# Kernel tuning notes

Measured on AMD Instinct MI355X. Metric: run time of the kernel, lower is better.

Reference implementation:

```python
import jax, jax.numpy as jnp
import numpy as np

D_MODEL = 2048
N_HEADS = 16
N_KV_HEADS = 4
D_K = D_MODEL // N_HEADS  # 128
N_REP = N_HEADS // N_KV_HEADS  # 4
EPS = 1e-8
ROPE_BASE = 10000.0


def setup_inputs() -> dict:
    key = jax.random.key(0)
    ks = jax.random.split(key, 6)
    B, S = 2, 2048
    s_in = 1.0 / np.sqrt(D_MODEL)
    return {
        "x": jax.random.normal(ks[0], (B, S, D_MODEL), jnp.float32),
        "Wq": jax.random.normal(ks[1], (D_MODEL, D_MODEL), jnp.float32) * s_in,
        "bq": jnp.zeros((D_MODEL,), jnp.float32),
        "Wk": jax.random.normal(ks[2], (N_KV_HEADS * D_K, D_MODEL), jnp.float32) * s_in,
        "bk": jnp.zeros((N_KV_HEADS * D_K,), jnp.float32),
        "Wv": jax.random.normal(ks[3], (N_KV_HEADS * D_K, D_MODEL), jnp.float32) * s_in,
        "bv": jnp.zeros((N_KV_HEADS * D_K,), jnp.float32),
        "Wo": jax.random.normal(ks[4], (D_MODEL, D_MODEL), jnp.float32) * s_in,
        "bo": jnp.zeros((D_MODEL,), jnp.float32),
        "q_norm_w": jnp.ones((D_K,), jnp.float32),
        "k_norm_w": jnp.ones((D_K,), jnp.float32),
    }


def _rmsnorm(x, w):
    rms = jnp.sqrt(jnp.mean(x * x, axis=-1, keepdims=True) + EPS)
    return x / rms * w


def _rope(x, cos, sin):
    # x: [B, S, H, d_k]; interleaved pair rotation (pairs along last dim)
    B, S, H, d = x.shape
    xr = x.reshape(B, S, H, d // 2, 2)
    x1, x2 = xr[..., 0], xr[..., 1]
    c = cos[:, None, :]  # [S, 1, d/2] -> broadcasts over [B, S, H, d/2]
    s = sin[:, None, :]
    o1 = x1 * c - x2 * s
    o2 = x1 * s + x2 * c
    return jnp.stack([o1, o2], axis=-1).reshape(B, S, H, d)


def reference(x, Wq, bq, Wk, bk, Wv, bv, Wo, bo, q_norm_w, k_norm_w):
    B, S, D = x.shape
    scale = 1.0 / np.sqrt(D_K)

    q = (x @ Wq.T + bq).reshape(B, S, N_HEADS, D_K)
    k = (x @ Wk.T + bk).reshape(B, S, N_KV_HEADS, D_K)
    v = (x @ Wv.T + bv).reshape(B, S, N_KV_HEADS, D_K)

    q = _rmsnorm(q, q_norm_w)
    k = _rmsnorm(k, k_norm_w)

    # RoPE tables (cos/sin of t * inv_freq), shape [S, d_k/2]
    inv_freq = 1.0 / (ROPE_BASE ** (jnp.arange(0, D_K, 2, dtype=jnp.float32) / D_K))
    freqs = jnp.arange(S, dtype=jnp.float32)[:, None] * inv_freq[None, :]
    cos, sin = jnp.cos(freqs), jnp.sin(freqs)
    q = _rope(q, cos, sin)
    k = _rope(k, cos, sin)

    # [B, H, S, d]
    q = q.transpose(0, 2, 1, 3)
    k = k.transpose(0, 2, 1, 3)
    v = v.transpose(0, 2, 1, 3)

    # GQA: group q heads by kv head instead of repeating k/v
    qg = q.reshape(B, N_KV_HEADS, N_REP, S, D_K)
    scores = jnp.einsum("bkrqd,bkld->bkrql", qg, k) * scale
    causal = jnp.tril(jnp.ones((S, S), dtype=bool))  # [S, S]
    scores = jnp.where(causal, scores, jnp.float32(-1e9))
    attn = jax.nn.softmax(scores, axis=-1)
    out = jnp.einsum("bkrql,bkld->bkrqd", attn, v)  # [B, Hk, rep, S, d]
    out = out.reshape(B, N_HEADS, S, D_K).transpose(0, 2, 1, 3).reshape(B, S, D)
    return out @ Wo.T + bo
```

## Files before the change

### kernel.cpp

```cpp
#include <hip/hip_runtime.h>
#include <hip/hip_bf16.h>
#include <stdint.h>

#define DM 2048
#define SQ 2048
#define NB 2
#define NH 16
#define NKV 4
#define DK 128
#define NQKV 3072

typedef unsigned short u16;
typedef unsigned int u32;
typedef __attribute__((ext_vector_type(8))) __bf16 bf16x8;
typedef __attribute__((ext_vector_type(4))) float f32x4;
typedef __attribute__((ext_vector_type(8))) u16 u16x8;
typedef __attribute__((ext_vector_type(2))) u32 u32x2;

__device__ __forceinline__ u16 f2bf(float f) {
  u32 x = __builtin_bit_cast(u32, f);
  x += 0x7fffu + ((x >> 16) & 1u);
  return (u16)(x >> 16);
}

__device__ __forceinline__ f32x4 mfma16(bf16x8 a, bf16x8 b, f32x4 c) {
  return __builtin_amdgcn_mfma_f32_16x16x32_bf16(a, b, c, 0, 0, 0);
}

#define GLDS16(g, l)                                                          \
  __builtin_amdgcn_global_load_lds(                                           \
      (const __attribute__((address_space(1))) void*)(g),                     \
      (__attribute__((address_space(3))) void*)(l), 16, 0, 0)

__global__ void cast_kernel(const float* __restrict__ src, u16* __restrict__ dst, int n8) {
  int i = blockIdx.x * blockDim.x + threadIdx.x;
  if (i >= n8) return;
  const float4* s4 = (const float4*)src;
  float4 a = s4[2 * i], b = s4[2 * i + 1];
  u16x8 v;
  v[0] = f2bf(a.x); v[1] = f2bf(a.y); v[2] = f2bf(a.z); v[3] = f2bf(a.w);
  v[4] = f2bf(b.x); v[5] = f2bf(b.y); v[6] = f2bf(b.z); v[7] = f2bf(b.w);
  *(u16x8*)(dst + 8 * (size_t)i) = v;
}

__global__ void fuse_bias(const float* __restrict__ bq, const float* __restrict__ bk,
                          const float* __restrict__ bv, float* __restrict__ fb) {
  int i = blockIdx.x * blockDim.x + threadIdx.x;
  if (i >= NQKV) return;
  float v;
  if (i < DM) v = bq[i];
  else if (i < DM + NKV * DK) v = bk[i - DM];
  else v = bv[i - DM - NKV * DK];
  fb[i] = v;
}

__global__ __launch_bounds__(256) void gemm_bt(
    const u16* __restrict__ A, const u16* __restrict__ W,
    const float* __restrict__ bias, float* __restrict__ C,
    int M, int N, int K) {
  __shared__ u16 As[128 * 64];
  __shared__ u16 Bs[128 * 64];
  const int tid = threadIdx.x;
  const int w = tid >> 6, l = tid & 63;
  const int hi = l >> 4, lo = l & 15;
  const int MB = M >> 7;
  const int nwg = gridDim.x;
  const int bid = blockIdx.x;
  const int swz = (bid & 7) * (nwg >> 3) + (bid >> 3);
  const int bm = swz % MB, bn = swz / MB;
  const int wr = w >> 1, wc = w & 1;
  const int lr8 = l >> 3, lc = l & 7;
  f32x4 acc[4][4] = {};
  for (int kt = 0; kt < K; kt += 64) {
#pragma unroll
    for (int i = 0; i < 4; ++i) {
      int row = w * 32 + i * 8 + lr8;
      int gc = lc ^ (row & 7);
      GLDS16(A + (size_t)(bm * 128 + row) * K + kt + gc * 8, &As[(w * 32 + i * 8) * 64]);
    }
#pragma unroll
    for (int i = 0; i < 4; ++i) {
      int row = w * 32 + i * 8 + lr8;
      int gc = lc ^ (row & 7);
      GLDS16(W + (size_t)(bn * 128 + row) * K + kt + gc * 8, &Bs[(w * 32 + i * 8) * 64]);
    }
    __syncthreads();
#pragma unroll
    for (int kk = 0; kk < 2; ++kk) {
      bf16x8 af[4], bf[4];
#pragma unroll
      for (int mi = 0; mi < 4; ++mi) {
        int row = wr * 64 + mi * 16 + lo;
        af[mi] = *(const bf16x8*)&As[row * 64 + (((kk * 4 + hi) ^ (row & 7)) * 8)];
      }
#pragma unroll
      for (int ni = 0; ni < 4; ++ni) {
        int row = wc * 64 + ni * 16 + lo;
        bf[ni] = *(const bf16x8*)&Bs[row * 64 + (((kk * 4 + hi) ^ (row & 7)) * 8)];
      }
#pragma unroll
      for (int mi = 0; mi < 4; ++mi)
#pragma unroll
        for (int ni = 0; ni < 4; ++ni)
          acc[mi][ni] = mfma16(af[mi], bf[ni], acc[mi][ni]);
    }
    __syncthreads();
  }
#pragma unroll
  for (int mi = 0; mi < 4; ++mi) {
#pragma unroll
    for (int ni = 0; ni < 4; ++ni) {
      int col = bn * 128 + wc * 64 + ni * 16 + lo;
      float bv = bias[col];
#pragma unroll
      for (int r = 0; r < 4; ++r) {
        int rowg = bm * 128 + wr * 64 + mi * 16 + hi * 4 + r;
        C[(size_t)rowg * N + col] = acc[mi][ni][r] + bv;
      }
    }
  }
}

__global__ void normrope_qk(const float* __restrict__ qkv,
                            const float* __restrict__ qw, const float* __restrict__ kw,
                            u16* __restrict__ qb, u16* __restrict__ kb) {
  int gw = (int)((blockIdx.x * (size_t)blockDim.x + threadIdx.x) >> 6);
  int lane = threadIdx.x & 63;
  int bs = gw / (NH + NKV), j = gw % (NH + NKV);
  int b = bs / SQ, s = bs % SQ;
  const float* src;
  const float* wgt;
  u16* dst;
  float post = 1.0f;
  if (j < NH) {
    src = qkv + (size_t)bs * NQKV + j * DK;
    wgt = qw;
    dst = qb + ((size_t)(b * NH + j) * SQ + s) * DK;
    post = 0.08838834764831845f;
  } else {
    int kh = j - NH;
    src = qkv + (size_t)bs * NQKV + DM + kh * DK;
    wgt = kw;
    dst = kb + ((size_t)(b * NKV + kh) * SQ + s) * DK;
  }
  float2 xv = *(const float2*)(src + 2 * lane);
  float ss = xv.x * xv.x + xv.y * xv.y;
#pragma unroll
  for (int m = 1; m < 64; m <<= 1) ss += __shfl_xor(ss, m);
  float inv = rsqrtf(ss * (1.0f / DK) + 1e-8f);
  float x1 = xv.x * inv * wgt[2 * lane];
  float x2 = xv.y * inv * wgt[2 * lane + 1];
  float theta = (float)s * expf((float)lane * (-9.2103403720f / 64.0f));
  float sn, cs;
  sincosf(theta, &sn, &cs);
  float o1 = (x1 * cs - x2 * sn) * post;
  float o2 = (x1 * sn + x2 * cs) * post;
  u32 pack = (u32)f2bf(o1) | ((u32)f2bf(o2) << 16);
  *(u32*)(dst + 2 * lane) = pack;
}

__global__ __launch_bounds__(256) void vtrans(const float* __restrict__ qkv, u16* __restrict__ vt) {
  __shared__ u16 T[128 * 72];
  int bid = blockIdx.x;
  int st = bid % (SQ / 64);
  int rem = bid / (SQ / 64);
  int vh = rem % NKV, b = rem / NKV;
  int s0 = st * 64;
  int t = threadIdx.x;
#pragma unroll
  for (int it = 0; it < 8; ++it) {
    int idx = it * 256 + t;
    int sl = idx >> 5;
    int c4 = idx & 31;
    float4 v = *(const float4*)(qkv + (size_t)(b * SQ + s0 + sl) * NQKV + DM + NKV * DK + vh * DK + c4 * 4);
    T[(c4 * 4 + 0) * 72 + sl] = f2bf(v.x);
    T[(c4 * 4 + 1) * 72 + sl] = f2bf(v.y);
    T[(c4 * 4 + 2) * 72 + sl] = f2bf(v.z);
    T[(c4 * 4 + 3) * 72 + sl] = f2bf(v.w);
  }
  __syncthreads();
#pragma unroll
  for (int it = 0; it < 4; ++it) {
    int idx = it * 256 + t;
    int d = idx >> 3;
    int ch = idx & 7;
    u16x8 v = *(const u16x8*)&T[d * 72 + ch * 8];
    *(u16x8*)(vt + ((size_t)(b * NKV + vh) * DK + d) * SQ + s0 + ch * 8) = v;
  }
}

__global__ __launch_bounds__(256) void attn(const u16* __restrict__ qb, const u16* __restrict__ kb,
                                            const u16* __restrict__ vt, u16* __restrict__ out) {
  __shared__ u16 Ks[2][64 * 128];
  __shared__ u16 Vs[2][128 * 64];
  __shared__ u16 P[4][16 * 64];
  const int w = threadIdx.x >> 6, l = threadIdx.x & 63;
  const int hi = l >> 4, lo = l & 15;
  const int pr = blockIdx.x, h = blockIdx.y, b = blockIdx.z;
  const int kvh = h >> 2;
  const u16* Q = qb + (size_t)(b * NH + h) * SQ * DK;
  const u16* K = kb + (size_t)(b * NKV + kvh) * SQ * DK;
  const u16* V = vt + (size_t)(b * NKV + kvh) * DK * SQ;

  auto stageKV = [&](int buf, int kt) {
#pragma unroll
    for (int i = 0; i < 4; ++i) {
      int rb = w * 16 + i * 4;
      int row = rb + (l >> 4);
      int gc = (l & 15) ^ (row & 7);
      GLDS16(K + (size_t)(kt + row) * DK + gc * 8, &Ks[buf][rb * 128]);
    }
#pragma unroll
    for (int i = 0; i < 4; ++i) {
      int rb = w * 32 + i * 8;
      int row = rb + (l >> 3);
      int gc = (l & 7) ^ (row & 7);
      GLDS16(V + (size_t)row * SQ + kt + gc * 8, &Vs[buf][rb * 64]);
    }
  };

#pragma unroll 1
  for (int seg = 0; seg < 2; ++seg) {
    const int qt = seg ? (SQ / 64 - 1 - pr) : pr;
    const int q0 = qt * 64 + w * 16;
    bf16x8 qf[4];
#pragma unroll
    for (int kk = 0; kk < 4; ++kk)
      qf[kk] = *(const bf16x8*)(Q + (size_t)(q0 + lo) * DK + kk * 32 + hi * 8);
    f32x4 oacc[8] = {};
    float lrun = 0.f;
    const int nt = qt + 1;
    stageKV(0, 0);
    __syncthreads();
#pragma unroll 1
    for (int ti = 0; ti < nt; ++ti) {
      const int cur = ti & 1;
      if (ti + 1 < nt) stageKV(cur ^ 1, (ti + 1) * 64);
      const int kt = ti * 64;
      f32x4 sfr[4];
      __builtin_amdgcn_s_setprio(1);
#pragma unroll
      for (int cb = 0; cb < 4; ++cb) {
        f32x4 sf = {};
#pragma unroll
        for (int kk = 0; kk < 4; ++kk) {
          int row = cb * 16 + lo;
          bf16x8 kfr = *(const bf16x8*)&Ks[cur][row * 128 + (((kk * 4 + hi) ^ (row & 7)) * 8)];
          sf = mfma16(kfr, qf[kk], sf);
        }
        sfr[cb] = sf;
      }
      __builtin_amdgcn_s_setprio(0);
      if (ti == nt - 1) {
#pragma unroll
        for (int cb = 0; cb < 4; ++cb)
#pragma unroll
          for (int r = 0; r < 4; ++r) {
            int kcol = kt + cb * 16 + hi * 4 + r;
            if (kcol > q0 + lo) sfr[cb][r] = -1e9f;
          }
      }
      float rs = 0.f;
#pragma unroll
      for (int cb = 0; cb < 4; ++cb) {
        float p0 = __expf(sfr[cb][0] - 12.0f);
        float p1 = __expf(sfr[cb][1] - 12.0f);
        float p2 = __expf(sfr[cb][2] - 12.0f);
        float p3 = __expf(sfr[cb][3] - 12.0f);
        rs += (p0 + p1) + (p2 + p3);
        u32x2 pw;
        pw[0] = (u32)f2bf(p0) | ((u32)f2bf(p1) << 16);
        pw[1] = (u32)f2bf(p2) | ((u32)f2bf(p3) << 16);
        int chunk = cb * 2 + (hi >> 1);
        *(u32x2*)&P[w][lo * 64 + ((chunk ^ (lo & 7)) * 8) + (hi & 1) * 4] = pw;
      }
      rs += __shfl_xor(rs, 16);
      rs += __shfl_xor(rs, 32);
      lrun += rs;
      __builtin_amdgcn_s_setprio(1);
#pragma unroll
      for (int half = 0; half < 2; ++half) {
        bf16x8 pa = *(const bf16x8*)&P[w][lo * 64 + (((half * 4 + hi) ^ (lo & 7)) * 8)];
#pragma unroll
        for (int fr = 0; fr < 8; ++fr) {
          int row = fr * 16 + lo;
          bf16x8 vfr = *(const bf16x8*)&Vs[cur][row * 64 + (((half * 4 + hi) ^ (row & 7)) * 8)];
          oacc[fr] = mfma16(pa, vfr, oacc[fr]);
        }
      }
      __builtin_amdgcn_s_setprio(0);
      __syncthreads();
    }
    float invl = 1.0f / lrun;
    float invlB[4];
#pragma unroll
    for (int r = 0; r < 4; ++r) invlB[r] = __shfl(invl, hi * 4 + r);
#pragma unroll
    for (int fr = 0; fr < 8; ++fr) {
#pragma unroll
      for (int r = 0; r < 4; ++r) {
        int row = b * SQ + q0 + hi * 4 + r;
        int col = h * DK + fr * 16 + lo;
        out[(size_t)row * DM + col] = f2bf(oacc[fr][r] * invlB[r]);
      }
    }
  }
}

extern "C" void kernel_launch(void* const* d_in, const int* in_sizes, int n_in,
                              void* d_out, int out_size, void* d_ws, size_t ws_size,
                              hipStream_t stream) {
  const float* x = (const float*)d_in[0];
  const float* Wq = (const float*)d_in[1];
  const float* bq = (const float*)d_in[2];
  const float* Wk = (const float*)d_in[3];
  const float* bk = (const float*)d_in[4];
  const float* Wv = (const float*)d_in[5];
  const float* bv = (const float*)d_in[6];
  const float* Wo = (const float*)d_in[7];
  const float* bo = (const float*)d_in[8];
  const float* qw = (const float*)d_in[9];
  const float* kw = (const float*)d_in[10];
  float* outp = (float*)d_out;

  char* ws = (char*)d_ws;
  size_t off = 0;
  auto alloc = [&](size_t bytes) {
    char* p = ws + off;
    off += (bytes + 255) & ~(size_t)255;
    return p;
  };
  u16* xb = (u16*)alloc((size_t)NB * SQ * DM * 2);
  u16* Wqkvb = (u16*)alloc((size_t)NQKV * DM * 2);
  u16* Wob = (u16*)alloc((size_t)DM * DM * 2);
  float* fbias = (float*)alloc((size_t)NQKV * 4);
  float* qkvf = (float*)alloc((size_t)NB * SQ * NQKV * 4);
  u16* qbh = (u16*)alloc((size_t)NB * NH * SQ * DK * 2);
  u16* kbh = (u16*)alloc((size_t)NB * NKV * SQ * DK * 2);
  u16* vth = (u16*)alloc((size_t)NB * NKV * DK * SQ * 2);
  u16* aout = (u16*)alloc((size_t)NB * SQ * DM * 2);

  {
    int n8 = NB * SQ * DM / 8;
    cast_kernel<<<(n8 + 255) / 256, 256, 0, stream>>>(x, xb, n8);
    n8 = DM * DM / 8;
    cast_kernel<<<(n8 + 255) / 256, 256, 0, stream>>>(Wq, Wqkvb, n8);
    cast_kernel<<<(n8 + 255) / 256, 256, 0, stream>>>(Wo, Wob, n8);
    n8 = NKV * DK * DM / 8;
    cast_kernel<<<(n8 + 255) / 256, 256, 0, stream>>>(Wk, Wqkvb + (size_t)DM * DM, n8);
    cast_kernel<<<(n8 + 255) / 256, 256, 0, stream>>>(Wv, Wqkvb + (size_t)(DM + NKV * DK) * DM, n8);
    fuse_bias<<<(NQKV + 255) / 256, 256, 0, stream>>>(bq, bk, bv, fbias);
  }
  {
    int M = NB * SQ;
    gemm_bt<<<(M / 128) * (NQKV / 128), 256, 0, stream>>>(xb, Wqkvb, fbias, qkvf, M, NQKV, DM);
  }
  {
    int waves = NB * SQ * (NH + NKV);
    normrope_qk<<<waves / 4, 256, 0, stream>>>(qkvf, qw, kw, qbh, kbh);
    vtrans<<<NB * NKV * (SQ / 64), 256, 0, stream>>>(qkvf, vth);
  }
  {
    dim3 g(SQ / 128, NH, NB);
    attn<<<g, 256, 0, stream>>>(qbh, kbh, vth, aout);
  }
  {
    int M = NB * SQ;
    gemm_bt<<<(M / 128) * (DM / 128), 256, 0, stream>>>(aout, Wob, bo, outp, M, DM, DM);
  }
}
```

Measured before the change: 235.8 us.

## Enlarge attention query tile, merge cast kernels, precompute RoPE table, drop GEMM swizzle

The attention kernel now has each wave handle two 16-row query groups, giving 128-row query tiles. Each staged K/V tile is therefore reused across twice as many queries. Causal masking is generalised per group, and fully masked tiles are skipped. The grid shrinks to 8 blocks per head and batch, which fewer blocks may leave some CUs idle. Separately, the five cast launches become one kernel, RoPE cos/sin come from a precomputed table, and the GEMM block-index swizzle is removed, which may hurt L2 locality.

```diff
diff --git a/kernel.cpp b/kernel.cpp
--- a/kernel.cpp
+++ b/kernel.cpp
@@ -32,15 +32,25 @@
       (const __attribute__((address_space(1))) void*)(g),                     \
       (__attribute__((address_space(3))) void*)(l), 16, 0, 0)
 
-__global__ void cast_kernel(const float* __restrict__ src, u16* __restrict__ dst, int n8) {
+__global__ void cast_all(const float* __restrict__ x, const float* __restrict__ Wq,
+                         const float* __restrict__ Wk, const float* __restrict__ Wv,
+                         const float* __restrict__ Wo, u16* __restrict__ xb,
+                         u16* __restrict__ Wqkvb, u16* __restrict__ Wob) {
   int i = blockIdx.x * blockDim.x + threadIdx.x;
-  if (i >= n8) return;
+  const float* src;
+  u16* dst;
+  int j;
+  if (i < 1048576) { src = x; dst = xb; j = i; }
+  else if (i < 1572864) { src = Wq; dst = Wqkvb; j = i - 1048576; }
+  else if (i < 1703936) { src = Wk; dst = Wqkvb + (size_t)DM * DM; j = i - 1572864; }
+  else if (i < 1835008) { src = Wv; dst = Wqkvb + (size_t)(DM + NKV * DK) * DM; j = i - 1703936; }
+  else { src = Wo; dst = Wob; j = i - 1835008; }
   const float4* s4 = (const float4*)src;
-  float4 a = s4[2 * i], b = s4[2 * i + 1];
+  float4 a = s4[2 * j], b = s4[2 * j + 1];
   u16x8 v;
   v[0] = f2bf(a.x); v[1] = f2bf(a.y); v[2] = f2bf(a.z); v[3] = f2bf(a.w);
   v[4] = f2bf(b.x); v[5] = f2bf(b.y); v[6] = f2bf(b.z); v[7] = f2bf(b.w);
-  *(u16x8*)(dst + 8 * (size_t)i) = v;
+  *(u16x8*)(dst + 8 * (size_t)j) = v;
 }
 
 __global__ void fuse_bias(const float* __restrict__ bq, const float* __restrict__ bk,
@@ -52,6 +62,16 @@
   else if (i < DM + NKV * DK) v = bk[i - DM];
   else v = bv[i - DM - NKV * DK];
   fb[i] = v;
+}
+
+__global__ void rope_table(float* __restrict__ ct, float* __restrict__ st_) {
+  int i = blockIdx.x * blockDim.x + threadIdx.x;
+  int s = i >> 6, d = i & 63;
+  float theta = (float)s * __expf((float)d * (-9.2103403720f / 64.0f));
+  float sn, cs;
+  sincosf(theta, &sn, &cs);
+  ct[i] = cs;
+  st_[i] = sn;
 }
 
 __global__ __launch_bounds__(256) void gemm_bt(
@@ -64,10 +84,7 @@
   const int w = tid >> 6, l = tid & 63;
   const int hi = l >> 4, lo = l & 15;
   const int MB = M >> 7;
-  const int nwg = gridDim.x;
-  const int bid = blockIdx.x;
-  const int swz = (bid & 7) * (nwg >> 3) + (bid >> 3);
-  const int bm = swz % MB, bn = swz / MB;
+  const int bm = blockIdx.x % MB, bn = blockIdx.x / MB;
   const int wr = w >> 1, wc = w & 1;
   const int lr8 = l >> 3, lc = l & 7;
   f32x4 acc[4][4] = {};
@@ -123,6 +140,7 @@
 
 __global__ void normrope_qk(const float* __restrict__ qkv,
                             const float* __restrict__ qw, const float* __restrict__ kw,
+                            const float* __restrict__ cosT, const float* __restrict__ sinT,
                             u16* __restrict__ qb, u16* __restrict__ kb) {
   int gw = (int)((blockIdx.x * (size_t)blockDim.x + threadIdx.x) >> 6);
   int lane = threadIdx.x & 63;
@@ -150,9 +168,8 @@
   float inv = rsqrtf(ss * (1.0f / DK) + 1e-8f);
   float x1 = xv.x * inv * wgt[2 * lane];
   float x2 = xv.y * inv * wgt[2 * lane + 1];
-  float theta = (float)s * expf((float)lane * (-9.2103403720f / 64.0f));
-  float sn, cs;
-  sincosf(theta, &sn, &cs);
+  float cs = cosT[s * 64 + lane];
+  float sn = sinT[s * 64 + lane];
   float o1 = (x1 * cs - x2 * sn) * post;
   float o2 = (x1 * sn + x2 * cs) * post;
   u32 pack = (u32)f2bf(o1) | ((u32)f2bf(o2) << 16);
@@ -193,7 +210,7 @@
                                             const u16* __restrict__ vt, u16* __restrict__ out) {
   __shared__ u16 Ks[2][64 * 128];
   __shared__ u16 Vs[2][128 * 64];
-  __shared__ u16 P[4][16 * 64];
+  __shared__ u16 P[8][16 * 64];
   const int w = threadIdx.x >> 6, l = threadIdx.x & 63;
   const int hi = l >> 4, lo = l & 15;
   const int pr = blockIdx.x, h = blockIdx.y, b = blockIdx.z;
@@ -221,15 +238,17 @@
 
 #pragma unroll 1
   for (int seg = 0; seg < 2; ++seg) {
-    const int qt = seg ? (SQ / 64 - 1 - pr) : pr;
-    const int q0 = qt * 64 + w * 16;
-    bf16x8 qf[4];
-#pragma unroll
-    for (int kk = 0; kk < 4; ++kk)
-      qf[kk] = *(const bf16x8*)(Q + (size_t)(q0 + lo) * DK + kk * 32 + hi * 8);
-    f32x4 oacc[8] = {};
-    float lrun = 0.f;
-    const int nt = qt + 1;
+    const int qt = seg ? (15 - pr) : pr;
+    const int qbase = qt * 128 + w * 32;
+    bf16x8 qf[2][4];
+#pragma unroll
+    for (int g = 0; g < 2; ++g)
+#pragma unroll
+      for (int kk = 0; kk < 4; ++kk)
+        qf[g][kk] = *(const bf16x8*)(Q + (size_t)(qbase + g * 16 + lo) * DK + kk * 32 + hi * 8);
+    f32x4 oacc[2][8] = {};
+    float lrun[2] = {0.f, 0.f};
+    const int nt = 2 * qt + 2;
     stageKV(0, 0);
     __syncthreads();
 #pragma unroll 1
@@ -237,71 +256,87 @@
       const int cur = ti & 1;
       if (ti + 1 < nt) stageKV(cur ^ 1, (ti + 1) * 64);
       const int kt = ti * 64;
-      f32x4 sfr[4];
-      __builtin_amdgcn_s_setprio(1);
-#pragma unroll
-      for (int cb = 0; cb < 4; ++cb) {
-        f32x4 sf = {};
-#pragma unroll
-        for (int kk = 0; kk < 4; ++kk) {
-          int row = cb * 16 + lo;
-          bf16x8 kfr = *(const bf16x8*)&Ks[cur][row * 128 + (((kk * 4 + hi) ^ (row & 7)) * 8)];
-          sf = mfma16(kfr, qf[kk], sf);
+      if (kt <= qbase + 31) {
+        f32x4 sfr[2][4];
+        __builtin_amdgcn_s_setprio(1);
+#pragma unroll
+        for (int cb = 0; cb < 4; ++cb) {
+          f32x4 sf0 = {}, sf1 = {};
+#pragma unroll
+          for (int kk = 0; kk < 4; ++kk) {
+            int row = cb * 16 + lo;
+            bf16x8 kfr = *(const bf16x8*)&Ks[cur][row * 128 + (((kk * 4 + hi) ^ (row & 7)) * 8)];
+            sf0 = mfma16(kfr, qf[0][kk], sf0);
+            sf1 = mfma16(kfr, qf[1][kk], sf1);
+          }
+          sfr[0][cb] = sf0;
+          sfr[1][cb] = sf1;
         }
-        sfr[cb] = sf;
+        __builtin_amdgcn_s_setprio(0);
+#pragma unroll
+        for (int g = 0; g < 2; ++g) {
+          int q0 = qbase + g * 16;
+          if (kt + 63 > q0) {
+#pragma unroll
+            for (int cb = 0; cb < 4; ++cb)
+#pragma unroll
+              for (int r = 0; r < 4; ++r) {
+                int kcol = kt + cb * 16 + hi * 4 + r;
+                if (kcol > q0 + lo) sfr[g][cb][r] = -1e9f;
+              }
+          }
+        }
+#pragma unroll
+        for (int g = 0; g < 2; ++g) {
+          float rs = 0.f;
+#pragma unroll
+          for (int cb = 0; cb < 4; ++cb) {
+            float p0 = __expf(sfr[g][cb][0] - 12.0f);
+            float p1 = __expf(sfr[g][cb][1] - 12.0f);
+            float p2 = __expf(sfr[g][cb][2] - 12.0f);
+            float p3 = __expf(sfr[g][cb][3] - 12.0f);
+            rs += (p0 + p1) + (p2 + p3);
+            u32x2 pw;
+            pw[0] = (u32)f2bf(p0) | ((u32)f2bf(p1) << 16);
+            pw[1] = (u32)f2bf(p2) | ((u32)f2bf(p3) << 16);
+            int chunk = cb * 2 + (hi >> 1);
+            *(u32x2*)&P[w * 2 + g][lo * 64 + ((chunk ^ (lo & 7)) * 8) + (hi & 1) * 4] = pw;
+          }
+          rs += __shfl_xor(rs, 16);
+          rs += __shfl_xor(rs, 32);
+          lrun[g] += rs;
+        }
+        __builtin_amdgcn_s_setprio(1);
+#pragma unroll
+        for (int half = 0; half < 2; ++half) {
+          bf16x8 pa0 = *(const bf16x8*)&P[w * 2 + 0][lo * 64 + (((half * 4 + hi) ^ (lo & 7)) * 8)];
+          bf16x8 pa1 = *(const bf16x8*)&P[w * 2 + 1][lo * 64 + (((half * 4 + hi) ^ (lo & 7)) * 8)];
+#pragma unroll
+          for (int fr = 0; fr < 8; ++fr) {
+            int row = fr * 16 + lo;
+            bf16x8 vfr = *(const bf16x8*)&Vs[cur][row * 64 + (((half * 4 + hi) ^ (row & 7)) * 8)];
+            oacc[0][fr] = mfma16(pa0, vfr, oacc[0][fr]);
+            oacc[1][fr] = mfma16(pa1, vfr, oacc[1][fr]);
+          }
+        }
+        __builtin_amdgcn_s_setprio(0);
       }
-      __builtin_amdgcn_s_setprio(0);
-      if (ti == nt - 1) {
-#pragma unroll
-        for (int cb = 0; cb < 4; ++cb)
-#pragma unroll
-          for (int r = 0; r < 4; ++r) {
-            int kcol = kt + cb * 16 + hi * 4 + r;
-            if (kcol > q0 + lo) sfr[cb][r] = -1e9f;
-          }
-      }
-      float rs = 0.f;
-#pragma unroll
-      for (int cb = 0; cb < 4; ++cb) {
-        float p0 = __expf(sfr[cb][0] - 12.0f);
-        float p1 = __expf(sfr[cb][1] - 12.0f);
-        float p2 = __expf(sfr[cb][2] - 12.0f);
-        float p3 = __expf(sfr[cb][3] - 12.0f);
-        rs += (p0 + p1) + (p2 + p3);
-        u32x2 pw;
-        pw[0] = (u32)f2bf(p0) | ((u32)f2bf(p1) << 16);
-        pw[1] = (u32)f2bf(p2) | ((u32)f2bf(p3) << 16);
-        int chunk = cb * 2 + (hi >> 1);
-        *(u32x2*)&P[w][lo * 64 + ((chunk ^ (lo & 7)) * 8) + (hi & 1) * 4] = pw;
-      }
-      rs += __shfl_xor(rs, 16);
-      rs += __shfl_xor(rs, 32);
-      lrun += rs;
-      __builtin_amdgcn_s_setprio(1);
-#pragma unroll
-      for (int half = 0; half < 2; ++half) {
-        bf16x8 pa = *(const bf16x8*)&P[w][lo * 64 + (((half * 4 + hi) ^ (lo & 7)) * 8)];
-#pragma unroll
-        for (int fr = 0; fr < 8; ++fr) {
-          int row = fr * 16 + lo;
-          bf16x8 vfr = *(const bf16x8*)&Vs[cur][row * 64 + (((half * 4 + hi) ^ (row & 7)) * 8)];
-          oacc[fr] = mfma16(pa, vfr, oacc[fr]);
+      __syncthreads();
+    }
+#pragma unroll
+    for (int g = 0; g < 2; ++g) {
+      float invl = 1.0f / lrun[g];
+      float invlB[4];
+#pragma unroll
+      for (int r = 0; r < 4; ++r) invlB[r] = __shfl(invl, hi * 4 + r);
+#pragma unroll
+      for (int fr = 0; fr < 8; ++fr) {
+#pragma unroll
+        for (int r = 0; r < 4; ++r) {
+          int row = b * SQ + qbase + g * 16 + hi * 4 + r;
+          int col = h * DK + fr * 16 + lo;
+          out[(size_t)row * DM + col] = f2bf(oacc[g][fr][r] * invlB[r]);
         }
-      }
-      __builtin_amdgcn_s_setprio(0);
-      __syncthreads();
-    }
-    float invl = 1.0f / lrun;
-    float invlB[4];
-#pragma unroll
-    for (int r = 0; r < 4; ++r) invlB[r] = __shfl(invl, hi * 4 + r);
-#pragma unroll
-    for (int fr = 0; fr < 8; ++fr) {
-#pragma unroll
-      for (int r = 0; r < 4; ++r) {
-        int row = b * SQ + q0 + hi * 4 + r;
-        int col = h * DK + fr * 16 + lo;
-        out[(size_t)row * DM + col] = f2bf(oacc[fr][r] * invlB[r]);
       }
     }
   }
@@ -334,34 +369,28 @@
   u16* Wqkvb = (u16*)alloc((size_t)NQKV * DM * 2);
   u16* Wob = (u16*)alloc((size_t)DM * DM * 2);
   float* fbias = (float*)alloc((size_t)NQKV * 4);
+  float* cosT = (float*)alloc((size_t)SQ * 64 * 4);
+  float* sinT = (float*)alloc((size_t)SQ * 64 * 4);
   float* qkvf = (float*)alloc((size_t)NB * SQ * NQKV * 4);
   u16* qbh = (u16*)alloc((size_t)NB * NH * SQ * DK * 2);
   u16* kbh = (u16*)alloc((size_t)NB * NKV * SQ * DK * 2);
   u16* vth = (u16*)alloc((size_t)NB * NKV * DK * SQ * 2);
   u16* aout = (u16*)alloc((size_t)NB * SQ * DM * 2);
 
-  {
-    int n8 = NB * SQ * DM / 8;
-    cast_kernel<<<(n8 + 255) / 256, 256, 0, stream>>>(x, xb, n8);
-    n8 = DM * DM / 8;
-    cast_kernel<<<(n8 + 255) / 256, 256, 0, stream>>>(Wq, Wqkvb, n8);
-    cast_kernel<<<(n8 + 255) / 256, 256, 0, stream>>>(Wo, Wob, n8);
-    n8 = NKV * DK * DM / 8;
-    cast_kernel<<<(n8 + 255) / 256, 256, 0, stream>>>(Wk, Wqkvb + (size_t)DM * DM, n8);
-    cast_kernel<<<(n8 + 255) / 256, 256, 0, stream>>>(Wv, Wqkvb + (size_t)(DM + NKV * DK) * DM, n8);
-    fuse_bias<<<(NQKV + 255) / 256, 256, 0, stream>>>(bq, bk, bv, fbias);
-  }
+  cast_all<<<2359296 / 256, 256, 0, stream>>>(x, Wq, Wk, Wv, Wo, xb, Wqkvb, Wob);
+  fuse_bias<<<(NQKV + 255) / 256, 256, 0, stream>>>(bq, bk, bv, fbias);
+  rope_table<<<(SQ * 64) / 256, 256, 0, stream>>>(cosT, sinT);
   {
     int M = NB * SQ;
     gemm_bt<<<(M / 128) * (NQKV / 128), 256, 0, stream>>>(xb, Wqkvb, fbias, qkvf, M, NQKV, DM);
   }
   {
     int waves = NB * SQ * (NH + NKV);
-    normrope_qk<<<waves / 4, 256, 0, stream>>>(qkvf, qw, kw, qbh, kbh);
+    normrope_qk<<<waves / 4, 256, 0, stream>>>(qkvf, qw, kw, cosT, sinT, qbh, kbh);
     vtrans<<<NB * NKV * (SQ / 64), 256, 0, stream>>>(qkvf, vth);
   }
   {
-    dim3 g(SQ / 128, NH, NB);
+    dim3 g(8, NH, NB);
     attn<<<g, 256, 0, stream>>>(qbh, kbh, vth, aout);
   }
   {
```

After: 243.5 us. +3.3%, slower.
